# Kernel optimization log

Measured on AMD Instinct MI355X. Metric: run time of the kernel, lower is better.

## Reference

```python
import jax, jax.numpy as jnp
import numpy as np
from jax import lax

B, C, H, W = 2, 64, 48, 48
NH, DK, DV = 8, 64, 128          # heads, per-head d_k, per-head d_v
DN, NS, R = 128, 16, 4           # SS2D d_inner (expand=2), d_state, dt_rank
MULT = 4                          # FFN expansion
L = H * W


def layer_norm(x, w, b, eps=1e-5):
    m = x.mean(-1, keepdims=True)
    v = ((x - m) ** 2).mean(-1, keepdims=True)
    return (x - m) / jnp.sqrt(v + eps) * w + b


def conv2d(x, w, groups=1):
    # x: NCHW, w: OIHW
    return lax.conv_general_dilated(x, w, (1, 1), 'SAME',
                                    dimension_numbers=('NCHW', 'OIHW', 'NCHW'),
                                    feature_group_count=groups)


def setup_inputs() -> dict:
    key = jax.random.key(0)
    ks = jax.random.split(key, 24)
    rn = lambda k, shp, s=0.02: jax.random.normal(k, shp, jnp.float32) * s
    inp = {
        'enc_input': jax.random.normal(ks[0], (B, C, H, W), jnp.float32),
        'slf_attn_snr': jax.random.uniform(ks[1], (B, 1, H, W), jnp.float32),
        # MultiHeadAttention params
        'attn_wq': rn(ks[2], (C, NH * DK)),
        'attn_wk': rn(ks[3], (C, NH * DK)),
        'attn_wv': rn(ks[4], (C, NH * DV)),
        'attn_fc': rn(ks[5], (NH * DV, C)),
        'attn_ln_w': jnp.ones((C,), jnp.float32),
        'attn_ln_b': jnp.zeros((C,), jnp.float32),
        # SS2D params
        'ss_in_w': rn(ks[6], (C, 2 * DN)),
        'ss_conv_w': rn(ks[7], (DN, 1, 3, 3)),
        'ss_conv_b': jnp.zeros((DN,), jnp.float32),
        'ss_xproj_w': rn(ks[8], (4, R + 2 * NS, DN)),
        'ss_dt_w': rn(ks[9], (4, DN, R)),
        'ss_dt_b': rn(ks[10], (4, DN)),
        'ss_Alog': jnp.log(jnp.broadcast_to(jnp.arange(1, NS + 1, dtype=jnp.float32), (4, DN, NS))),
        'ss_D': jnp.ones((4, DN), jnp.float32),
        'ss_norm_w': jnp.ones((DN,), jnp.float32),
        'ss_norm_b': jnp.zeros((DN,), jnp.float32),
        'ss_out_w': rn(ks[11], (DN, C)),
        # FFN (PreNorm + conv block)
        'ffn_ln_w': jnp.ones((C,), jnp.float32),
        'ffn_ln_b': jnp.zeros((C,), jnp.float32),
        'ffn_w1': rn(ks[12], (C * MULT, C, 1, 1)),
        'ffn_dw': rn(ks[13], (C * MULT, 1, 3, 3)),
        'ffn_w2': rn(ks[14], (C, C * MULT, 1, 1)),
    }
    return inp


def reference(enc_input, slf_attn_snr, attn_wq, attn_wk, attn_wv, attn_fc,
              attn_ln_w, attn_ln_b, ss_in_w, ss_conv_w, ss_conv_b, ss_xproj_w,
              ss_dt_w, ss_dt_b, ss_Alog, ss_D, ss_norm_w, ss_norm_b, ss_out_w,
              ffn_ln_w, ffn_ln_b, ffn_w1, ffn_dw, ffn_w2):
    # ---- Multi-head self-attention over spatial tokens (SNR-biased) ----
    x_tok = enc_input.reshape(B, C, L).transpose(0, 2, 1)        # (B, L, C)
    q = (x_tok @ attn_wq).reshape(B, L, NH, DK).transpose(0, 2, 1, 3)
    k = (x_tok @ attn_wk).reshape(B, L, NH, DK).transpose(0, 2, 1, 3)
    v = (x_tok @ attn_wv).reshape(B, L, NH, DV).transpose(0, 2, 1, 3)
    scores = jnp.einsum('bhqd,bhkd->bhqk', q, k) / jnp.sqrt(jnp.float32(DK))
    snr_flat = slf_attn_snr.reshape(B, 1, 1, L)                  # bias over keys
    scores = scores + jnp.log(snr_flat + 1e-4)
    attn = jax.nn.softmax(scores, axis=-1)                       # (B, NH, L, L)
    o = jnp.einsum('bhqk,bhkd->bhqd', attn, v)
    o = o.transpose(0, 2, 1, 3).reshape(B, L, NH * DV) @ attn_fc
    enc_output = layer_norm(o + x_tok, attn_ln_w, attn_ln_b)     # post-LN residual
    enc_output = enc_output.transpose(0, 2, 1).reshape(B, C, H, W)

    # ---- SS2D: 4-direction 2D selective scan ----
    xh = enc_output.transpose(0, 2, 3, 1)                        # (B, H, W, C)
    snr_h = slf_attn_snr.transpose(0, 2, 3, 1)                   # (B, H, W, 1)
    xz = xh @ ss_in_w                                            # (B, H, W, 2*DN)
    x1, z = xz[..., :DN], xz[..., DN:]
    x1 = x1.transpose(0, 3, 1, 2)                                # (B, DN, H, W)
    x1 = conv2d(x1, ss_conv_w, groups=DN) + ss_conv_b[None, :, None, None]
    x1 = jax.nn.silu(x1)

    x_hw = x1.reshape(B, DN, L)
    x_wh = x1.transpose(0, 1, 3, 2).reshape(B, DN, L)
    xs = jnp.stack([x_hw, x_wh], axis=1)                         # (B, 2, DN, L)
    xs = jnp.concatenate([xs, jnp.flip(xs, axis=-1)], axis=1)    # (B, 4, DN, L)

    x_dbl = jnp.einsum('bkdl,kcd->bkcl', xs, ss_xproj_w)
    dts, Bs, Cs = x_dbl[:, :, :R], x_dbl[:, :, R:R + NS], x_dbl[:, :, R + NS:]
    dts = jnp.einsum('bkrl,kdr->bkdl', dts, ss_dt_w) + ss_dt_b[None, :, :, None]
    dts = jax.nn.softplus(dts)                                   # (B, 4, DN, L)
    A = -jnp.exp(ss_Alog)                                        # (4, DN, NS)

    def step(h, inp):
        xt, dtt, Bt, Ct = inp                                    # (B,4,DN),(B,4,DN),(B,4,NS),(B,4,NS)
        dA = jnp.exp(dtt[..., None] * A)                         # (B,4,DN,NS)
        h = h * dA + (dtt * xt)[..., None] * Bt[:, :, None, :]
        y = jnp.einsum('bkdn,bkn->bkd', h, Ct)
        return h, y

    h0 = jnp.zeros((B, 4, DN, NS), jnp.float32)
    elems = (xs.transpose(3, 0, 1, 2), dts.transpose(3, 0, 1, 2),
             Bs.transpose(3, 0, 1, 2), Cs.transpose(3, 0, 1, 2))
    _, ys = lax.scan(step, h0, elems)                            # (L, B, 4, DN)
    ys = ys.transpose(1, 2, 3, 0) + ss_D[None, :, :, None] * xs  # (B, 4, DN, L)

    inv = jnp.flip(ys[:, 2:4], axis=-1)                          # undo reversed scans
    wh = ys[:, 1].reshape(B, DN, W, H).transpose(0, 1, 3, 2).reshape(B, DN, L)
    invwh = inv[:, 1].reshape(B, DN, W, H).transpose(0, 1, 3, 2).reshape(B, DN, L)
    y = ys[:, 0] + inv[:, 0] + wh + invwh                        # (B, DN, L)
    y = y.transpose(0, 2, 1).reshape(B, H, W, DN)
    y = layer_norm(y, ss_norm_w, ss_norm_b) * jax.nn.silu(z) * snr_h
    x2 = y @ ss_out_w + enc_input.transpose(0, 2, 3, 1)          # (B, H, W, C)

    # ---- PreNorm conv FeedForward ----
    xn = layer_norm(x2, ffn_ln_w, ffn_ln_b).transpose(0, 3, 1, 2)
    h1 = jax.nn.gelu(conv2d(xn, ffn_w1), approximate=False)
    h1 = jax.nn.gelu(conv2d(h1, ffn_dw, groups=C * MULT), approximate=False)
    h1 = conv2d(h1, ffn_w2).transpose(0, 2, 3, 1)
    x3 = h1 + x2

    return x3.transpose(0, 3, 1, 2)                              # (B, C, H, W)
```

## Files before the change

kernel.cpp:

```cpp
#include <hip/hip_runtime.h>
#include <hip/hip_bf16.h>

#define Bq 2
#define Cc 64
#define Hh 48
#define Ww 48
#define Ll 2304
#define NHh 8
#define DKk 64
#define DVv 128
#define DNn 128
#define NSs 16
#define Rr 4
#define SCH 48
#define SNC 48
#define TT 8

#define OQ    0u
#define OK_   2359296u
#define OV    4718592u
#define OO    9437184u
#define OY2   14450688u
#define OX2   15040512u
#define OXN   15335424u
#define OVT   15630336u
#define WS_NEED_FLOATS (OVT + 4718592u)
#define ODT2  OQ
#define OYS2  OK_
#define OX1P  OV
#define OZ    (OV + 589824u)
#define OX1S  (OV + 1179648u)
#define OBS2  (OV + 1769472u)
#define OCS2  (OV + 2064384u)
#define OCSA  (OV + 2359296u)
#define OCSB  (OV + 3145728u)
#define OHST  (OV + 3932160u)
#define OH1A  OO
#define OH1B  (OO + 1179648u)

typedef short short8v __attribute__((ext_vector_type(8)));
typedef short short4v __attribute__((ext_vector_type(4)));
typedef float f32x4 __attribute__((ext_vector_type(4)));
typedef unsigned short ushort_t;

__device__ __forceinline__ float geluf(float x) {
  return 0.5f * x * (1.0f + erff(x * 0.70710678118654752f));
}
__device__ __forceinline__ float siluf(float x) {
  return x / (1.0f + __expf(-x));
}
__device__ __forceinline__ float softplusf(float x) {
  return fmaxf(x, 0.0f) + log1pf(__expf(-fabsf(x)));
}
__device__ __forceinline__ int spmap(int k, int l) {
  if (k == 0) return l;
  if (k == 1) return (l % 48) * 48 + l / 48;
  if (k == 2) return 2303 - l;
  int l2 = 2303 - l; return (l2 % 48) * 48 + l2 / 48;
}
__device__ __forceinline__ short f2bf(float f) {
  unsigned u = __float_as_uint(f);
  unsigned r = (u + 0x7FFFu + ((u >> 16) & 1u)) >> 16;
  return (short)r;
}

__global__ void k_code(float* out) { if (threadIdx.x == 0) out[0] = 25000.f; }

__global__ __launch_bounds__(256) void k_qkv(const float* __restrict__ enc,
    const float* __restrict__ wq, const float* __restrict__ wk,
    const float* __restrict__ wv, float* __restrict__ ws) {
  int l0 = blockIdx.x * TT; int b = blockIdx.y;
  int t = threadIdx.x;
  __shared__ float xs[64][12];
  {
    int idx = t, c = idx >> 3, i = idx & 7;
    xs[c][i] = enc[(size_t)b * Cc * Ll + (size_t)c * Ll + l0 + i];
    idx = t + 256; c = idx >> 3; i = idx & 7;
    xs[c][i] = enc[(size_t)b * Cc * Ll + (size_t)c * Ll + l0 + i];
  }
  __syncthreads();
  ushort_t* qb = (ushort_t*)(ws + OQ);
  ushort_t* kb = (ushort_t*)(ws + OK_);
  float* v = ws + OV;
#pragma unroll
  for (int g = 0; g < 6; ++g) {
    int j = t + g * 256;
    float acc[TT];
#pragma unroll
    for (int i = 0; i < TT; ++i) acc[i] = 0.f;
    const float* wp; int col, stride;
    if (j < 512) { wp = wq + j; stride = 512; col = j; }
    else if (j < 1024) { wp = wk + (j - 512); stride = 512; col = j - 512; }
    else { wp = wv + (j - 1024); stride = 1024; col = j - 1024; }
    for (int c = 0; c < 64; ++c) {
      float w = wp[(size_t)c * stride];
      const float4* xc = (const float4*)&xs[c][0];
      float4 x0 = xc[0], x1 = xc[1];
      acc[0] += x0.x * w; acc[1] += x0.y * w;
      acc[2] += x0.z * w; acc[3] += x0.w * w;
      acc[4] += x1.x * w; acc[5] += x1.y * w;
      acc[6] += x1.z * w; acc[7] += x1.w * w;
    }
    if (j < 512) {
#pragma unroll
      for (int i = 0; i < TT; ++i)
        qb[((size_t)(b * 8 + (col >> 6)) * Ll + l0 + i) * 64 + (col & 63)] =
            (ushort_t)f2bf(acc[i] * 0.125f);
    } else if (j < 1024) {
#pragma unroll
      for (int i = 0; i < TT; ++i)
        kb[((size_t)(b * 8 + (col >> 6)) * Ll + l0 + i) * 64 + (col & 63)] =
            (ushort_t)f2bf(acc[i]);
    } else {
#pragma unroll
      for (int i = 0; i < TT; ++i)
        v[((size_t)(b * 8 + (col >> 7)) * Ll + l0 + i) * 128 + (col & 127)] = acc[i];
    }
  }
}

__global__ __launch_bounds__(256) void k_vt(float* __restrict__ ws) {
  int bh = blockIdx.y;
  int l0 = blockIdx.x * 64;
  int t = threadIdx.x;
  __shared__ float tile[128][65];
  const float* vp = ws + OV + ((size_t)bh * Ll + l0) * 128;
  for (int i = t; i < 64 * 32; i += 256) {
    int l = i >> 5, dv4 = (i & 31) * 4;
    float4 a = *(const float4*)(vp + (size_t)l * 128 + dv4);
    tile[dv4][l] = a.x; tile[dv4 + 1][l] = a.y;
    tile[dv4 + 2][l] = a.z; tile[dv4 + 3][l] = a.w;
  }
  __syncthreads();
  ushort_t* vt = (ushort_t*)(ws + OVT) + (size_t)bh * 128 * Ll + l0;
  for (int i = t; i < 128 * 16; i += 256) {
    int dv = i >> 4, l4 = (i & 15) * 4;
    short4v a;
    a[0] = f2bf(tile[dv][l4]); a[1] = f2bf(tile[dv][l4 + 1]);
    a[2] = f2bf(tile[dv][l4 + 2]); a[3] = f2bf(tile[dv][l4 + 3]);
    *(short4v*)(vt + (size_t)dv * Ll + l4) = a;
  }
}

#define NKT 36
#define LSK 72
__global__ __launch_bounds__(256) void k_attn(const float* __restrict__ snr,
                                              float* __restrict__ ws) {
  int bh = blockIdx.y; int b = bh >> 3; int hd = bh & 7;
  int q0 = blockIdx.x * 64;
  int t = threadIdx.x;
  int w = t >> 6, lane = t & 63;
  int m16 = lane & 15, quad = lane >> 4;

  __shared__ __align__(16) ushort_t Ks[64 * LSK];
  __shared__ __align__(16) ushort_t Vs[128 * LSK];
  __shared__ __align__(16) ushort_t Ps[4 * 16 * LSK];
  __shared__ float sfac_s[64];
  __shared__ float lsc[4][16];

  const ushort_t* qbf = (const ushort_t*)(ws + OQ) + (size_t)bh * Ll * 64;
  const ushort_t* kbf = (const ushort_t*)(ws + OK_) + (size_t)bh * Ll * 64;
  const ushort_t* vtb = (const ushort_t*)(ws + OVT) + (size_t)bh * 128 * Ll;

  short8v qa[2];
  {
    const ushort_t* qrp = qbf + (size_t)(q0 + w * 16 + m16) * 64 + quad * 8;
    qa[0] = *(const short8v*)qrp;
    qa[1] = *(const short8v*)(qrp + 32);
  }
  int sk_key = t >> 2, sk_d0 = (t & 3) * 16;
  int sv_dv = t >> 1, sv_k0 = (t & 1) * 32;

  short8v kreg[2], vreg[4];
  float snr_reg = 0.f;
  {
    const ushort_t* ksrc = kbf + (size_t)sk_key * 64 + sk_d0;
    kreg[0] = *(const short8v*)ksrc;
    kreg[1] = *(const short8v*)(ksrc + 8);
    const ushort_t* vsrc = vtb + (size_t)sv_dv * Ll + sv_k0;
#pragma unroll
    for (int i = 0; i < 4; ++i) vreg[i] = *(const short8v*)(vsrc + i * 8);
    if (t < 64) snr_reg = snr[b * Ll + t];
  }

  f32x4 oacc[8];
#pragma unroll
  for (int i = 0; i < 8; ++i) oacc[i] = (f32x4)0.f;
  float l_r[4] = {0.f, 0.f, 0.f, 0.f};

  for (int kt = 0; kt < NKT; ++kt) {
    __syncthreads();
    *(short8v*)&Ks[sk_key * LSK + sk_d0] = kreg[0];
    *(short8v*)&Ks[sk_key * LSK + sk_d0 + 8] = kreg[1];
#pragma unroll
    for (int i = 0; i < 4; ++i)
      *(short8v*)&Vs[sv_dv * LSK + sv_k0 + i * 8] = vreg[i];
    if (t < 64) sfac_s[t] = snr_reg + 1e-4f;
    __syncthreads();
    if (kt + 1 < NKT) {
      int k0n = (kt + 1) * 64;
      const ushort_t* ksrc = kbf + (size_t)(k0n + sk_key) * 64 + sk_d0;
      kreg[0] = *(const short8v*)ksrc;
      kreg[1] = *(const short8v*)(ksrc + 8);
      const ushort_t* vsrc = vtb + (size_t)sv_dv * Ll + k0n + sv_k0;
#pragma unroll
      for (int i = 0; i < 4; ++i) vreg[i] = *(const short8v*)(vsrc + i * 8);
      if (t < 64) snr_reg = snr[b * Ll + k0n + t];
    }

    f32x4 sac[4];
#pragma unroll
    for (int n = 0; n < 4; ++n) {
      int key = n * 16 + m16;
      short8v kb0 = *(const short8v*)&Ks[key * LSK + quad * 8];
      short8v kb1 = *(const short8v*)&Ks[key * LSK + 32 + quad * 8];
      f32x4 acc = (f32x4)0.f;
      acc = __builtin_amdgcn_mfma_f32_16x16x32_bf16(qa[0], kb0, acc, 0, 0, 0);
      acc = __builtin_amdgcn_mfma_f32_16x16x32_bf16(qa[1], kb1, acc, 0, 0, 0);
      sac[n] = acc;
    }
    float sf[4];
#pragma unroll
    for (int n = 0; n < 4; ++n) sf[n] = sfac_s[n * 16 + m16];
    ushort_t* pw = &Ps[w * 16 * LSK];
#pragma unroll
    for (int r = 0; r < 4; ++r) {
#pragma unroll
      for (int n = 0; n < 4; ++n) {
        float p = __expf(sac[n][r]) * sf[n];
        l_r[r] += p;
        pw[(quad * 4 + r) * LSK + n * 16 + m16] = (ushort_t)f2bf(p);
      }
    }
    short8v pb0 = *(const short8v*)&pw[m16 * LSK + quad * 8];
    short8v pb1 = *(const short8v*)&pw[m16 * LSK + 32 + quad * 8];
#pragma unroll
    for (int dt_ = 0; dt_ < 8; ++dt_) {
      const ushort_t* vrow = &Vs[(dt_ * 16 + m16) * LSK];
      short8v va0 = *(const short8v*)&vrow[quad * 8];
      short8v va1 = *(const short8v*)&vrow[32 + quad * 8];
      f32x4 o = oacc[dt_];
      o = __builtin_amdgcn_mfma_f32_16x16x32_bf16(va0, pb0, o, 0, 0, 0);
      o = __builtin_amdgcn_mfma_f32_16x16x32_bf16(va1, pb1, o, 0, 0, 0);
      oacc[dt_] = o;
    }
  }
#pragma unroll
  for (int r = 0; r < 4; ++r) {
    float lv = l_r[r];
    lv += __shfl_xor(lv, 1, 64);
    lv += __shfl_xor(lv, 2, 64);
    lv += __shfl_xor(lv, 4, 64);
    lv += __shfl_xor(lv, 8, 64);
    l_r[r] = lv;
  }
  if (m16 == 0) {
#pragma unroll
    for (int r = 0; r < 4; ++r) lsc[w][quad * 4 + r] = l_r[r];
  }
  float linv = 1.f / lsc[w][m16];
  float* op = ws + OO + ((size_t)(b * Ll + q0 + w * 16 + m16)) * 1024 + hd * 128;
#pragma unroll
  for (int dt_ = 0; dt_ < 8; ++dt_) {
#pragma unroll
    for (int r = 0; r < 4; ++r) {
      op[dt_ * 16 + quad * 4 + r] = oacc[dt_][r] * linv;
    }
  }
}

__global__ __launch_bounds__(256) void k_oprojxz(const float* __restrict__ enc,
    const float* __restrict__ fc, const float* __restrict__ lnw,
    const float* __restrict__ lnb, const float* __restrict__ ssin,
    float* __restrict__ ws) {
  int l0 = blockIdx.x * TT, b = blockIdx.y, t = threadIdx.x;
  __shared__ float orow[1024][9];
  __shared__ float part[4][TT][64];
  __shared__ float xh_s[64][9];
  const float* op = ws + OO + ((size_t)(b * Ll + l0)) * 1024;
#pragma unroll
  for (int k = 0; k < 4; ++k) {
    int c = t + k * 256;
#pragma unroll
    for (int i = 0; i < TT; ++i) orow[c][i] = op[(size_t)i * 1024 + c];
  }
  __syncthreads();
  int col = t & 63, seg = t >> 6;
  {
    float acc[TT];
#pragma unroll
    for (int i = 0; i < TT; ++i) acc[i] = 0.f;
    const float* fcs = fc + (size_t)(seg * 256) * 64 + col;
    for (int c = 0; c < 256; ++c) {
      float w = fcs[(size_t)c * 64];
      const float* orc = &orow[seg * 256 + c][0];
#pragma unroll
      for (int i = 0; i < TT; ++i) acc[i] += orc[i] * w;
    }
#pragma unroll
    for (int i = 0; i < TT; ++i) part[seg][i][col] = acc[i];
  }
  __syncthreads();
  if (t < 64) {
    float lw = lnw[t], lb = lnb[t];
#pragma unroll
    for (int i = 0; i < TT; ++i) {
      float a = part[0][i][t] + part[1][i][t] + part[2][i][t] + part[3][i][t];
      a += enc[(size_t)b * Cc * Ll + (size_t)t * Ll + l0 + i];
      float s = a;
#pragma unroll
      for (int o = 32; o >= 1; o >>= 1) s += __shfl_xor(s, o, 64);
      float m = s * (1.f / 64.f);
      float dd = a - m;
      float vs = dd * dd;
#pragma unroll
      for (int o = 32; o >= 1; o >>= 1) vs += __shfl_xor(vs, o, 64);
      xh_s[t][i] = dd * rsqrtf(vs * (1.f / 64.f) + 1e-5f) * lw + lb;
    }
  }
  __syncthreads();
  {
    float acc2[TT];
#pragma unroll
    for (int i = 0; i < TT; ++i) acc2[i] = 0.f;
    for (int c = 0; c < 64; ++c) {
      float w = ssin[c * 256 + t];
      const float* xc = &xh_s[c][0];
#pragma unroll
      for (int i = 0; i < TT; ++i) acc2[i] += xc[i] * w;
    }
    if (t < 128) {
#pragma unroll
      for (int i = 0; i < TT; ++i)
        ws[OX1P + ((size_t)(b * Ll + l0 + i)) * 128 + t] = acc2[i];
    } else {
#pragma unroll
      for (int i = 0; i < TT; ++i)
        ws[OZ + ((size_t)(b * Ll + l0 + i)) * 128 + (t - 128)] = acc2[i];
    }
  }
}

__global__ __launch_bounds__(128) void k_conv(const float* __restrict__ cw,
    const float* __restrict__ cb, float* __restrict__ ws) {
  int l = blockIdx.x, b = blockIdx.y, d = threadIdx.x;
  int h = l / 48, w = l % 48;
  float acc = cb[d];
#pragma unroll
  for (int kh = 0; kh < 3; ++kh) {
    int hh = h + kh - 1;
    if (hh < 0 || hh >= 48) continue;
#pragma unroll
    for (int kw = 0; kw < 3; ++kw) {
      int wx = w + kw - 1;
      if (wx < 0 || wx >= 48) continue;
      acc += ws[OX1P + ((size_t)b * Ll + hh * 48 + wx) * 128 + d] *
             cw[d * 9 + kh * 3 + kw];
    }
  }
  ws[OX1S + ((size_t)b * Ll + l) * 128 + d] = siluf(acc);
}

__global__ __launch_bounds__(128) void k_xdbl(const float* __restrict__ xw,
    const float* __restrict__ dtw, const float* __restrict__ dtb,
    float* __restrict__ ws) {
  int l0 = blockIdx.x * TT;
  int by = blockIdx.y; int b = by >> 2; int k = by & 3;
  int t = threadIdx.x;
  __shared__ float xv[128][9];
  __shared__ float pr[36][TT];
#pragma unroll
  for (int i = 0; i < TT; ++i) {
    int sp = spmap(k, l0 + i);
    xv[t][i] = ws[OX1S + ((size_t)(b * Ll) + sp) * 128 + t];
  }
  __syncthreads();
  if (t < 36) {
    float s[TT];
#pragma unroll
    for (int i = 0; i < TT; ++i) s[i] = 0.f;
    const float* wp = xw + (size_t)(k * 36 + t) * 128;
    for (int d = 0; d < 128; ++d) {
      float w = wp[d];
      const float* xc = &xv[d][0];
#pragma unroll
      for (int i = 0; i < TT; ++i) s[i] += xc[i] * w;
    }
#pragma unroll
    for (int i = 0; i < TT; ++i) pr[t][i] = s[i];
  }
  __syncthreads();
  {
    int d = t;
    const float* wp = dtw + (size_t)(k * 128 + d) * 4;
    float w0 = wp[0], w1 = wp[1], w2 = wp[2], w3 = wp[3];
    float bb = dtb[k * 128 + d];
#pragma unroll
    for (int i = 0; i < TT; ++i) {
      float v = pr[0][i] * w0 + pr[1][i] * w1 + pr[2][i] * w2 + pr[3][i] * w3 + bb;
      ws[ODT2 + ((size_t)(by * Ll + l0 + i)) * 128 + d] = softplusf(v);
    }
  }
  if (t < 16) {
#pragma unroll
    for (int i = 0; i < TT; ++i)
      ws[OBS2 + ((size_t)(by * Ll + l0 + i)) * 16 + t] = pr[4 + t][i];
  } else if (t < 32) {
#pragma unroll
    for (int i = 0; i < TT; ++i)
      ws[OCS2 + ((size_t)(by * Ll + l0 + i)) * 16 + (t - 16)] = pr[20 + (t - 16)][i];
  }
}

__global__ __launch_bounds__(256) void k_scanA(const float* __restrict__ alog,
                                               float* __restrict__ ws) {
  int c = blockIdx.x;
  int bk = blockIdx.y;
  int b = bk >> 2, k = bk & 3;
  int t = threadIdx.x;
  int n = t & 15, dg = t >> 4;
  __shared__ float dt_s[128], x_s[128], Bs_s[16];
  float A_r[8], ap[8], bc[8];
#pragma unroll
  for (int i = 0; i < 8; ++i) {
    int d = dg * 8 + i;
    A_r[i] = -__expf(alog[(size_t)((k * 128 + d) * 16) + n]);
    ap[i] = 1.f; bc[i] = 0.f;
  }
  const float* dtp = ws + ODT2 + ((size_t)bk * Ll) * 128;
  const float* bsp = ws + OBS2 + ((size_t)bk * Ll) * 16;
  const float* xb = ws + OX1S + (size_t)b * Ll * 128;
  for (int ll = 0; ll < SCH; ++ll) {
    int l = c * SCH + ll;
    int sp = spmap(k, l);
    if (t < 128) dt_s[t] = dtp[(size_t)l * 128 + t];
    else x_s[t - 128] = xb[(size_t)sp * 128 + (t - 128)];
    if (t < 16) Bs_s[t] = bsp[(size_t)l * 16 + t];
    __syncthreads();
    float Bv = Bs_s[n];
#pragma unroll
    for (int i = 0; i < 8; ++i) {
      int d = dg * 8 + i;
      float dtv = dt_s[d];
      float a = __expf(dtv * A_r[i]);
      bc[i] = bc[i] * a + dtv * x_s[d] * Bv;
      ap[i] *= a;
    }
    __syncthreads();
  }
  float* csa = ws + OCSA + ((size_t)(bk * SNC + c) * 128) * 16;
  float* csb = ws + OCSB + ((size_t)(bk * SNC + c) * 128) * 16;
#pragma unroll
  for (int i = 0; i < 8; ++i) {
    int d = dg * 8 + i;
    csa[d * 16 + n] = ap[i];
    csb[d * 16 + n] = bc[i];
  }
}

__global__ __launch_bounds__(256) void k_scanB(float* __restrict__ ws) {
  int g = blockIdx.x * 256 + threadIdx.x;
  int bk = g >> 11;
  int dn = g & 2047;
  const float* csa = ws + OCSA;
  const float* csb = ws + OCSB;
  float* hst = ws + OHST;
  float h = 0.f;
  for (int c = 0; c < SNC; ++c) {
    size_t idx = (size_t)(bk * SNC + c) * 2048 + dn;
    hst[idx] = h;
    h = csa[idx] * h + csb[idx];
  }
}

__global__ __launch_bounds__(256) void k_scanC(const float* __restrict__ alog,
    const float* __restrict__ Dp, float* __restrict__ ws) {
  int c = blockIdx.x, bk = blockIdx.y;
  int b = bk >> 2, k = bk & 3;
  int t = threadIdx.x;
  int n = t & 15, dg = t >> 4;
  __shared__ float dt_s[128], x_s[128], Bs_s[16], Cs_s[16];
  float A_r[8], h[8], Dv[8];
#pragma unroll
  for (int i = 0; i < 8; ++i) {
    int d = dg * 8 + i;
    A_r[i] = -__expf(alog[(size_t)((k * 128 + d) * 16) + n]);
    h[i] = ws[OHST + ((size_t)(bk * SNC + c) * 128 + d) * 16 + n];
    Dv[i] = Dp[k * 128 + d];
  }
  const float* dtp = ws + ODT2 + ((size_t)bk * Ll) * 128;
  const float* bsp = ws + OBS2 + ((size_t)bk * Ll) * 16;
  const float* csp = ws + OCS2 + ((size_t)bk * Ll) * 16;
  const float* xb = ws + OX1S + (size_t)b * Ll * 128;
  float* yp = ws + OYS2 + ((size_t)bk * Ll) * 128;
  for (int ll = 0; ll < SCH; ++ll) {
    int l = c * SCH + ll;
    int sp = spmap(k, l);
    if (t < 128) dt_s[t] = dtp[(size_t)l * 128 + t];
    else x_s[t - 128] = xb[(size_t)sp * 128 + (t - 128)];
    if (t < 16) Bs_s[t] = bsp[(size_t)l * 16 + t];
    else if (t < 32) Cs_s[t - 16] = csp[(size_t)l * 16 + (t - 16)];
    __syncthreads();
    float Bv = Bs_s[n], Cv = Cs_s[n];
    float yacc[8];
#pragma unroll
    for (int i = 0; i < 8; ++i) {
      int d = dg * 8 + i;
      float dtv = dt_s[d];
      float a = __expf(dtv * A_r[i]);
      h[i] = h[i] * a + dtv * x_s[d] * Bv;
      yacc[i] = h[i] * Cv;
    }
#pragma unroll
    for (int i = 0; i < 8; ++i) {
      float yv = yacc[i];
      yv += __shfl_xor(yv, 1, 64);
      yv += __shfl_xor(yv, 2, 64);
      yv += __shfl_xor(yv, 4, 64);
      yv += __shfl_xor(yv, 8, 64);
      yacc[i] = yv;
    }
    if (n == 0) {
#pragma unroll
      for (int i = 0; i < 8; ++i) {
        int d = dg * 8 + i;
        yp[(size_t)l * 128 + d] = yacc[i] + Dv[i] * x_s[d];
      }
    }
    __syncthreads();
  }
}

__global__ __launch_bounds__(128) void k_comb(const float* __restrict__ nw,
    const float* __restrict__ nb, const float* __restrict__ snr,
    float* __restrict__ ws) {
  int l = blockIdx.x, b = blockIdx.y, d = threadIdx.x;
  int h = l / 48, w = l % 48;
  int lT = w * 48 + h;
  const float* ysb = ws + OYS2;
  float v = ysb[((size_t)(b * 4 + 0) * Ll + l) * 128 + d] +
            ysb[((size_t)(b * 4 + 2) * Ll + (2303 - l)) * 128 + d] +
            ysb[((size_t)(b * 4 + 1) * Ll + lT) * 128 + d] +
            ysb[((size_t)(b * 4 + 3) * Ll + (2303 - lT)) * 128 + d];
  __shared__ float red[4];
  int lane = d & 63, wid = d >> 6;
  float s = v;
#pragma unroll
  for (int o = 32; o >= 1; o >>= 1) s += __shfl_xor(s, o, 64);
  if (lane == 0) red[wid] = s;
  __syncthreads();
  float m = (red[0] + red[1]) * (1.f / 128.f);
  float dv_ = v - m;
  float q = dv_ * dv_;
#pragma unroll
  for (int o = 32; o >= 1; o >>= 1) q += __shfl_xor(q, o, 64);
  if (lane == 0) red[wid + 2] = q;
  __syncthreads();
  float var = (red[2] + red[3]) * (1.f / 128.f);
  float y = dv_ * rsqrtf(var + 1e-5f) * nw[d] + nb[d];
  float zv = ws[OZ + ((size_t)b * Ll + l) * 128 + d];
  y *= siluf(zv);
  y *= snr[b * Ll + l];
  ws[OY2 + ((size_t)b * Ll + l) * 128 + d] = y;
}

__global__ __launch_bounds__(256) void k_outffn1(const float* __restrict__ enc,
    const float* __restrict__ ow, const float* __restrict__ lw,
    const float* __restrict__ lb, const float* __restrict__ w1,
    float* __restrict__ ws) {
  int l0 = blockIdx.x * TT, b = blockIdx.y, t = threadIdx.x;
  __shared__ float yr[128][9];
  __shared__ float part[2][TT][64];
  __shared__ float xn_s[64][9];
  const float* yp = ws + OY2 + ((size_t)(b * Ll + l0)) * 128;
  if (t < 128) {
#pragma unroll
    for (int i = 0; i < TT; ++i) yr[t][i] = yp[(size_t)i * 128 + t];
  }
  __syncthreads();
  if (t < 128) {
    int col = t & 63, seg = t >> 6;
    float acc[TT];
#pragma unroll
    for (int i = 0; i < TT; ++i) acc[i] = 0.f;
    const float* ows = ow + (size_t)(seg * 64) * 64 + col;
    for (int c = 0; c < 64; ++c) {
      float w = ows[c * 64];
      const float* yc = &yr[seg * 64 + c][0];
#pragma unroll
      for (int i = 0; i < TT; ++i) acc[i] += yc[i] * w;
    }
#pragma unroll
    for (int i = 0; i < TT; ++i) part[seg][i][col] = acc[i];
  }
  __syncthreads();
  if (t < 64) {
    float lwv = lw[t], lbv = lb[t];
#pragma unroll
    for (int i = 0; i < TT; ++i) {
      float a = part[0][i][t] + part[1][i][t];
      a += enc[(size_t)b * Cc * Ll + (size_t)t * Ll + l0 + i];
      ws[OX2 + ((size_t)(b * Ll + l0 + i)) * 64 + t] = a;
      float s = a;
#pragma unroll
      for (int o = 32; o >= 1; o >>= 1) s += __shfl_xor(s, o, 64);
      float m = s * (1.f / 64.f);
      float dd2 = a - m;
      float vs = dd2 * dd2;
#pragma unroll
      for (int o = 32; o >= 1; o >>= 1) vs += __shfl_xor(vs, o, 64);
      xn_s[t][i] = dd2 * rsqrtf(vs * (1.f / 64.f) + 1e-5f) * lwv + lbv;
    }
  }
  __syncthreads();
  {
    float acc2[TT];
#pragma unroll
    for (int i = 0; i < TT; ++i) acc2[i] = 0.f;
    const float* wp = w1 + (size_t)t * 64;
    for (int c = 0; c < 64; ++c) {
      float w = wp[c];
      const float* xc = &xn_s[c][0];
#pragma unroll
      for (int i = 0; i < TT; ++i) acc2[i] += xc[i] * w;
    }
#pragma unroll
    for (int i = 0; i < TT; ++i)
      ws[OH1A + ((size_t)(b * Ll + l0 + i)) * 256 + t] = geluf(acc2[i]);
  }
}

__global__ __launch_bounds__(256) void k_ffndw(const float* __restrict__ dww,
                                               float* __restrict__ ws) {
  int l = blockIdx.x, b = blockIdx.y, mch = threadIdx.x;
  int h = l / 48, w = l % 48;
  float acc = 0.f;
#pragma unroll
  for (int kh = 0; kh < 3; ++kh) {
    int hh = h + kh - 1;
    if (hh < 0 || hh >= 48) continue;
#pragma unroll
    for (int kw = 0; kw < 3; ++kw) {
      int wx = w + kw - 1;
      if (wx < 0 || wx >= 48) continue;
      acc += ws[OH1A + ((size_t)b * Ll + hh * 48 + wx) * 256 + mch] *
             dww[mch * 9 + kh * 3 + kw];
    }
  }
  ws[OH1B + ((size_t)b * Ll + l) * 256 + mch] = geluf(acc);
}

__global__ __launch_bounds__(256) void k_ffn2(const float* __restrict__ w2,
                                              float* __restrict__ ws,
                                              float* __restrict__ out) {
  int l0 = blockIdx.x * TT, b = blockIdx.y, t = threadIdx.x;
  __shared__ float hr[256][9];
  __shared__ float part[4][TT][64];
  const float* hp = ws + OH1B + ((size_t)(b * Ll + l0)) * 256;
#pragma unroll
  for (int i = 0; i < TT; ++i) hr[t][i] = hp[(size_t)i * 256 + t];
  __syncthreads();
  int col = t & 63, seg = t >> 6;
  {
    float acc[TT];
#pragma unroll
    for (int i = 0; i < TT; ++i) acc[i] = 0.f;
    const float* wp = w2 + (size_t)col * 256 + seg * 64;
    for (int c = 0; c < 64; ++c) {
      float w = wp[c];
      const float* hc = &hr[seg * 64 + c][0];
#pragma unroll
      for (int i = 0; i < TT; ++i) acc[i] += hc[i] * w;
    }
#pragma unroll
    for (int i = 0; i < TT; ++i) part[seg][i][col] = acc[i];
  }
  __syncthreads();
  if (t < 64) {
    float av[TT];
#pragma unroll
    for (int i = 0; i < TT; ++i) {
      float a = part[0][i][t] + part[1][i][t] + part[2][i][t] + part[3][i][t];
      av[i] = a + ws[OX2 + ((size_t)(b * Ll + l0 + i)) * 64 + t];
    }
    float* opx = out + ((size_t)(b * 64 + t)) * 2304 + l0;
    *(float4*)opx = make_float4(av[0], av[1], av[2], av[3]);
    *((float4*)opx + 1) = make_float4(av[4], av[5], av[6], av[7]);
  }
}

extern "C" void kernel_launch(void* const* d_in, const int* in_sizes, int n_in,
                              void* d_out, int out_size, void* d_ws, size_t ws_size,
                              hipStream_t stream) {
  (void)in_sizes; (void)n_in; (void)out_size;
  const float* enc  = (const float*)d_in[0];
  const float* snr  = (const float*)d_in[1];
  const float* wq   = (const float*)d_in[2];
  const float* wk   = (const float*)d_in[3];
  const float* wv   = (const float*)d_in[4];
  const float* fc   = (const float*)d_in[5];
  const float* alnw = (const float*)d_in[6];
  const float* alnb = (const float*)d_in[7];
  const float* ssin = (const float*)d_in[8];
  const float* cw   = (const float*)d_in[9];
  const float* cb   = (const float*)d_in[10];
  const float* xw   = (const float*)d_in[11];
  const float* dtw  = (const float*)d_in[12];
  const float* dtb  = (const float*)d_in[13];
  const float* alog = (const float*)d_in[14];
  const float* Dp   = (const float*)d_in[15];
  const float* nw   = (const float*)d_in[16];
  const float* nb   = (const float*)d_in[17];
  const float* ow   = (const float*)d_in[18];
  const float* flnw = (const float*)d_in[19];
  const float* flnb = (const float*)d_in[20];
  const float* w1   = (const float*)d_in[21];
  const float* dww  = (const float*)d_in[22];
  const float* w2   = (const float*)d_in[23];
  float* ws = (float*)d_ws;
  float* out = (float*)d_out;

  if (ws_size < (size_t)WS_NEED_FLOATS * 4) {
    hipLaunchKernelGGL(k_code, dim3(1), dim3(64), 0, stream, out);
    return;
  }

  hipLaunchKernelGGL(k_qkv, dim3(Ll / TT, Bq), dim3(256), 0, stream, enc, wq, wk, wv, ws);
  hipLaunchKernelGGL(k_vt, dim3(Ll / 64, Bq * NHh), dim3(256), 0, stream, ws);
  hipLaunchKernelGGL(k_attn, dim3(Ll / 64, Bq * NHh), dim3(256), 0, stream, snr, ws);
  hipLaunchKernelGGL(k_oprojxz, dim3(Ll / TT, Bq), dim3(256), 0, stream, enc, fc, alnw, alnb, ssin, ws);
  hipLaunchKernelGGL(k_conv, dim3(Ll, Bq), dim3(128), 0, stream, cw, cb, ws);
  hipLaunchKernelGGL(k_xdbl, dim3(Ll / TT, Bq * 4), dim3(128), 0, stream, xw, dtw, dtb, ws);
  hipLaunchKernelGGL(k_scanA, dim3(SNC, Bq * 4), dim3(256), 0, stream, alog, ws);
  hipLaunchKernelGGL(k_scanB, dim3(64), dim3(256), 0, stream, ws);
  hipLaunchKernelGGL(k_scanC, dim3(SNC, Bq * 4), dim3(256), 0, stream, alog, Dp, ws);
  hipLaunchKernelGGL(k_comb, dim3(Ll, Bq), dim3(128), 0, stream, nw, nb, snr, ws);
  hipLaunchKernelGGL(k_outffn1, dim3(Ll / TT, Bq), dim3(256), 0, stream, enc, ow, flnw, flnb, w1, ws);
  hipLaunchKernelGGL(k_ffndw, dim3(Ll, Bq), dim3(256), 0, stream, dww, ws);
  hipLaunchKernelGGL(k_ffn2, dim3(Ll / TT, Bq), dim3(256), 0, stream, w2, ws, out);
}
```

Measured before the change: 461.2 us.

## Tile depthwise convs in shared memory, prefetch scan inputs, fuse combine into FFN1

```diff
diff --git a/kernel.cpp b/kernel.cpp
--- a/kernel.cpp
+++ b/kernel.cpp
@@ -341,24 +341,37 @@
   }
 }
 
-__global__ __launch_bounds__(128) void k_conv(const float* __restrict__ cw,
+__global__ __launch_bounds__(256) void k_conv(const float* __restrict__ cw,
     const float* __restrict__ cb, float* __restrict__ ws) {
-  int l = blockIdx.x, b = blockIdx.y, d = threadIdx.x;
-  int h = l / 48, w = l % 48;
-  float acc = cb[d];
-#pragma unroll
-  for (int kh = 0; kh < 3; ++kh) {
-    int hh = h + kh - 1;
-    if (hh < 0 || hh >= 48) continue;
-#pragma unroll
-    for (int kw = 0; kw < 3; ++kw) {
-      int wx = w + kw - 1;
-      if (wx < 0 || wx >= 48) continue;
-      acc += ws[OX1P + ((size_t)b * Ll + hh * 48 + wx) * 128 + d] *
-             cw[d * 9 + kh * 3 + kw];
-    }
-  }
-  ws[OX1S + ((size_t)b * Ll + l) * 128 + d] = siluf(acc);
+  int l0 = blockIdx.x * TT, b = blockIdx.y, t = threadIdx.x;
+  int h = l0 / 48, w0 = l0 % 48;
+  __shared__ float tile[3][10][128];
+  for (int idx = t; idx < 3840; idx += 256) {
+    int r = idx / 1280, rem = idx % 1280;
+    int col = rem >> 7, d = rem & 127;
+    int hh = h + r - 1, wx = w0 + col - 1;
+    float v = 0.f;
+    if (hh >= 0 && hh < 48 && wx >= 0 && wx < 48)
+      v = ws[OX1P + ((size_t)(b * Ll + hh * 48 + wx)) * 128 + d];
+    tile[r][col][d] = v;
+  }
+  __syncthreads();
+  int d = t & 127, half = t >> 7;
+  float cwr[9];
+#pragma unroll
+  for (int j = 0; j < 9; ++j) cwr[j] = cw[d * 9 + j];
+  float cbv = cb[d];
+#pragma unroll
+  for (int j = 0; j < 4; ++j) {
+    int i = half * 4 + j;
+    float acc = cbv;
+#pragma unroll
+    for (int kh = 0; kh < 3; ++kh)
+#pragma unroll
+      for (int kw = 0; kw < 3; ++kw)
+        acc += tile[kh][i + kw][d] * cwr[kh * 3 + kw];
+    ws[OX1S + ((size_t)(b * Ll + l0 + i)) * 128 + d] = siluf(acc);
+  }
 }
 
 __global__ __launch_bounds__(128) void k_xdbl(const float* __restrict__ xw,
@@ -430,13 +443,27 @@
   const float* dtp = ws + ODT2 + ((size_t)bk * Ll) * 128;
   const float* bsp = ws + OBS2 + ((size_t)bk * Ll) * 16;
   const float* xb = ws + OX1S + (size_t)b * Ll * 128;
+  float r_a = 0.f, r_Bs = 0.f;
+  {
+    int l = c * SCH;
+    int sp = spmap(k, l);
+    if (t < 128) r_a = dtp[(size_t)l * 128 + t];
+    else r_a = xb[(size_t)sp * 128 + (t - 128)];
+    if (t < 16) r_Bs = bsp[(size_t)l * 16 + t];
+  }
   for (int ll = 0; ll < SCH; ++ll) {
-    int l = c * SCH + ll;
-    int sp = spmap(k, l);
-    if (t < 128) dt_s[t] = dtp[(size_t)l * 128 + t];
-    else x_s[t - 128] = xb[(size_t)sp * 128 + (t - 128)];
-    if (t < 16) Bs_s[t] = bsp[(size_t)l * 16 + t];
     __syncthreads();
+    if (t < 128) dt_s[t] = r_a;
+    else x_s[t - 128] = r_a;
+    if (t < 16) Bs_s[t] = r_Bs;
+    __syncthreads();
+    if (ll + 1 < SCH) {
+      int l2 = c * SCH + ll + 1;
+      int sp2 = spmap(k, l2);
+      if (t < 128) r_a = dtp[(size_t)l2 * 128 + t];
+      else r_a = xb[(size_t)sp2 * 128 + (t - 128)];
+      if (t < 16) r_Bs = bsp[(size_t)l2 * 16 + t];
+    }
     float Bv = Bs_s[n];
 #pragma unroll
     for (int i = 0; i < 8; ++i) {
@@ -446,7 +473,6 @@
       bc[i] = bc[i] * a + dtv * x_s[d] * Bv;
       ap[i] *= a;
     }
-    __syncthreads();
   }
   float* csa = ws + OCSA + ((size_t)(bk * SNC + c) * 128) * 16;
   float* csb = ws + OCSB + ((size_t)(bk * SNC + c) * 128) * 16;
@@ -493,14 +519,31 @@
   const float* csp = ws + OCS2 + ((size_t)bk * Ll) * 16;
   const float* xb = ws + OX1S + (size_t)b * Ll * 128;
   float* yp = ws + OYS2 + ((size_t)bk * Ll) * 128;
+  float r_a = 0.f, r_bc = 0.f;
+  {
+    int l = c * SCH;
+    int sp = spmap(k, l);
+    if (t < 128) r_a = dtp[(size_t)l * 128 + t];
+    else r_a = xb[(size_t)sp * 128 + (t - 128)];
+    if (t < 16) r_bc = bsp[(size_t)l * 16 + t];
+    else if (t < 32) r_bc = csp[(size_t)l * 16 + (t - 16)];
+  }
   for (int ll = 0; ll < SCH; ++ll) {
+    __syncthreads();
+    if (t < 128) dt_s[t] = r_a;
+    else x_s[t - 128] = r_a;
+    if (t < 16) Bs_s[t] = r_bc;
+    else if (t < 32) Cs_s[t - 16] = r_bc;
+    __syncthreads();
+    if (ll + 1 < SCH) {
+      int l2 = c * SCH + ll + 1;
+      int sp2 = spmap(k, l2);
+      if (t < 128) r_a = dtp[(size_t)l2 * 128 + t];
+      else r_a = xb[(size_t)sp2 * 128 + (t - 128)];
+      if (t < 16) r_bc = bsp[(size_t)l2 * 16 + t];
+      else if (t < 32) r_bc = csp[(size_t)l2 * 16 + (t - 16)];
+    }
     int l = c * SCH + ll;
-    int sp = spmap(k, l);
-    if (t < 128) dt_s[t] = dtp[(size_t)l * 128 + t];
-    else x_s[t - 128] = xb[(size_t)sp * 128 + (t - 128)];
-    if (t < 16) Bs_s[t] = bsp[(size_t)l * 16 + t];
-    else if (t < 32) Cs_s[t - 16] = csp[(size_t)l * 16 + (t - 16)];
-    __syncthreads();
     float Bv = Bs_s[n], Cv = Cs_s[n];
     float yacc[8];
 #pragma unroll
@@ -527,55 +570,78 @@
         yp[(size_t)l * 128 + d] = yacc[i] + Dv[i] * x_s[d];
       }
     }
-    __syncthreads();
-  }
-}
-
-__global__ __launch_bounds__(128) void k_comb(const float* __restrict__ nw,
-    const float* __restrict__ nb, const float* __restrict__ snr,
-    float* __restrict__ ws) {
-  int l = blockIdx.x, b = blockIdx.y, d = threadIdx.x;
-  int h = l / 48, w = l % 48;
-  int lT = w * 48 + h;
-  const float* ysb = ws + OYS2;
-  float v = ysb[((size_t)(b * 4 + 0) * Ll + l) * 128 + d] +
-            ysb[((size_t)(b * 4 + 2) * Ll + (2303 - l)) * 128 + d] +
-            ysb[((size_t)(b * 4 + 1) * Ll + lT) * 128 + d] +
-            ysb[((size_t)(b * 4 + 3) * Ll + (2303 - lT)) * 128 + d];
-  __shared__ float red[4];
-  int lane = d & 63, wid = d >> 6;
-  float s = v;
-#pragma unroll
-  for (int o = 32; o >= 1; o >>= 1) s += __shfl_xor(s, o, 64);
-  if (lane == 0) red[wid] = s;
-  __syncthreads();
-  float m = (red[0] + red[1]) * (1.f / 128.f);
-  float dv_ = v - m;
-  float q = dv_ * dv_;
-#pragma unroll
-  for (int o = 32; o >= 1; o >>= 1) q += __shfl_xor(q, o, 64);
-  if (lane == 0) red[wid + 2] = q;
-  __syncthreads();
-  float var = (red[2] + red[3]) * (1.f / 128.f);
-  float y = dv_ * rsqrtf(var + 1e-5f) * nw[d] + nb[d];
-  float zv = ws[OZ + ((size_t)b * Ll + l) * 128 + d];
-  y *= siluf(zv);
-  y *= snr[b * Ll + l];
-  ws[OY2 + ((size_t)b * Ll + l) * 128 + d] = y;
-}
-
-__global__ __launch_bounds__(256) void k_outffn1(const float* __restrict__ enc,
-    const float* __restrict__ ow, const float* __restrict__ lw,
-    const float* __restrict__ lb, const float* __restrict__ w1,
-    float* __restrict__ ws) {
+  }
+}
+
+__global__ __launch_bounds__(256) void k_combffn1(const float* __restrict__ enc,
+    const float* __restrict__ nw, const float* __restrict__ nb,
+    const float* __restrict__ snr, const float* __restrict__ ow,
+    const float* __restrict__ lw, const float* __restrict__ lb,
+    const float* __restrict__ w1, float* __restrict__ ws) {
   int l0 = blockIdx.x * TT, b = blockIdx.y, t = threadIdx.x;
   __shared__ float yr[128][9];
+  __shared__ float redm[2][TT], redq[2][TT];
   __shared__ float part[2][TT][64];
   __shared__ float xn_s[64][9];
-  const float* yp = ws + OY2 + ((size_t)(b * Ll + l0)) * 128;
+  int lane = t & 63, wid = (t >> 6) & 1;
+  float v[TT], m[TT];
   if (t < 128) {
-#pragma unroll
-    for (int i = 0; i < TT; ++i) yr[t][i] = yp[(size_t)i * 128 + t];
+    int d = t;
+    const float* ysb = ws + OYS2;
+#pragma unroll
+    for (int i = 0; i < TT; ++i) {
+      int l = l0 + i;
+      int hh = l / 48, wwp = l % 48;
+      int lT = wwp * 48 + hh;
+      v[i] = ysb[((size_t)(b * 4 + 0) * Ll + l) * 128 + d] +
+             ysb[((size_t)(b * 4 + 2) * Ll + (2303 - l)) * 128 + d] +
+             ysb[((size_t)(b * 4 + 1) * Ll + lT) * 128 + d] +
+             ysb[((size_t)(b * 4 + 3) * Ll + (2303 - lT)) * 128 + d];
+    }
+    float s[TT];
+#pragma unroll
+    for (int i = 0; i < TT; ++i) s[i] = v[i];
+#pragma unroll
+    for (int o = 32; o >= 1; o >>= 1)
+#pragma unroll
+      for (int i = 0; i < TT; ++i) s[i] += __shfl_xor(s[i], o, 64);
+    if (lane == 0) {
+#pragma unroll
+      for (int i = 0; i < TT; ++i) redm[wid][i] = s[i];
+    }
+  }
+  __syncthreads();
+  if (t < 128) {
+    float q[TT];
+#pragma unroll
+    for (int i = 0; i < TT; ++i) {
+      m[i] = (redm[0][i] + redm[1][i]) * (1.f / 128.f);
+      float dv = v[i] - m[i];
+      q[i] = dv * dv;
+    }
+#pragma unroll
+    for (int o = 32; o >= 1; o >>= 1)
+#pragma unroll
+      for (int i = 0; i < TT; ++i) q[i] += __shfl_xor(q[i], o, 64);
+    if (lane == 0) {
+#pragma unroll
+      for (int i = 0; i < TT; ++i) redq[wid][i] = q[i];
+    }
+  }
+  __syncthreads();
+  if (t < 128) {
+    int d = t;
+    float nwv = nw[d], nbv = nb[d];
+#pragma unroll
+    for (int i = 0; i < TT; ++i) {
+      int l = l0 + i;
+      float var = (redq[0][i] + redq[1][i]) * (1.f / 128.f);
+      float y = (v[i] - m[i]) * rsqrtf(var + 1e-5f) * nwv + nbv;
+      float zv = ws[OZ + ((size_t)(b * Ll + l)) * 128 + d];
+      y *= siluf(zv);
+      y *= snr[b * Ll + l];
+      yr[d][i] = y;
+    }
   }
   __syncthreads();
   if (t < 128) {
@@ -604,8 +670,8 @@
       float s = a;
 #pragma unroll
       for (int o = 32; o >= 1; o >>= 1) s += __shfl_xor(s, o, 64);
-      float m = s * (1.f / 64.f);
-      float dd2 = a - m;
+      float mm = s * (1.f / 64.f);
+      float dd2 = a - mm;
       float vs = dd2 * dd2;
 #pragma unroll
       for (int o = 32; o >= 1; o >>= 1) vs += __shfl_xor(vs, o, 64);
@@ -632,22 +698,32 @@
 
 __global__ __launch_bounds__(256) void k_ffndw(const float* __restrict__ dww,
                                                float* __restrict__ ws) {
-  int l = blockIdx.x, b = blockIdx.y, mch = threadIdx.x;
-  int h = l / 48, w = l % 48;
-  float acc = 0.f;
-#pragma unroll
-  for (int kh = 0; kh < 3; ++kh) {
-    int hh = h + kh - 1;
-    if (hh < 0 || hh >= 48) continue;
-#pragma unroll
-    for (int kw = 0; kw < 3; ++kw) {
-      int wx = w + kw - 1;
-      if (wx < 0 || wx >= 48) continue;
-      acc += ws[OH1A + ((size_t)b * Ll + hh * 48 + wx) * 256 + mch] *
-             dww[mch * 9 + kh * 3 + kw];
-    }
-  }
-  ws[OH1B + ((size_t)b * Ll + l) * 256 + mch] = geluf(acc);
+  int l0 = blockIdx.x * TT, b = blockIdx.y, t = threadIdx.x;
+  int h = l0 / 48, w0 = l0 % 48;
+  __shared__ float tile[3][10][256];
+  for (int idx = t; idx < 7680; idx += 256) {
+    int r = idx / 2560, rem = idx % 2560;
+    int col = rem >> 8, ch = rem & 255;
+    int hh = h + r - 1, wx = w0 + col - 1;
+    float v = 0.f;
+    if (hh >= 0 && hh < 48 && wx >= 0 && wx < 48)
+      v = ws[OH1A + ((size_t)(b * Ll + hh * 48 + wx)) * 256 + ch];
+    tile[r][col][ch] = v;
+  }
+  __syncthreads();
+  float dwr[9];
+#pragma unroll
+  for (int j = 0; j < 9; ++j) dwr[j] = dww[t * 9 + j];
+#pragma unroll
+  for (int i = 0; i < TT; ++i) {
+    float acc = 0.f;
+#pragma unroll
+    for (int kh = 0; kh < 3; ++kh)
+#pragma unroll
+      for (int kw = 0; kw < 3; ++kw)
+        acc += tile[kh][i + kw][t] * dwr[kh * 3 + kw];
+    ws[OH1B + ((size_t)(b * Ll + l0 + i)) * 256 + t] = geluf(acc);
+  }
 }
 
 __global__ __launch_bounds__(256) void k_ffn2(const float* __restrict__ w2,
@@ -729,13 +805,12 @@
   hipLaunchKernelGGL(k_vt, dim3(Ll / 64, Bq * NHh), dim3(256), 0, stream, ws);
   hipLaunchKernelGGL(k_attn, dim3(Ll / 64, Bq * NHh), dim3(256), 0, stream, snr, ws);
   hipLaunchKernelGGL(k_oprojxz, dim3(Ll / TT, Bq), dim3(256), 0, stream, enc, fc, alnw, alnb, ssin, ws);
-  hipLaunchKernelGGL(k_conv, dim3(Ll, Bq), dim3(128), 0, stream, cw, cb, ws);
+  hipLaunchKernelGGL(k_conv, dim3(Ll / TT, Bq), dim3(256), 0, stream, cw, cb, ws);
   hipLaunchKernelGGL(k_xdbl, dim3(Ll / TT, Bq * 4), dim3(128), 0, stream, xw, dtw, dtb, ws);
   hipLaunchKernelGGL(k_scanA, dim3(SNC, Bq * 4), dim3(256), 0, stream, alog, ws);
   hipLaunchKernelGGL(k_scanB, dim3(64), dim3(256), 0, stream, ws);
   hipLaunchKernelGGL(k_scanC, dim3(SNC, Bq * 4), dim3(256), 0, stream, alog, Dp, ws);
-  hipLaunchKernelGGL(k_comb, dim3(Ll, Bq), dim3(128), 0, stream, nw, nb, snr, ws);
-  hipLaunchKernelGGL(k_outffn1, dim3(Ll / TT, Bq), dim3(256), 0, stream, enc, ow, flnw, flnb, w1, ws);
-  hipLaunchKernelGGL(k_ffndw, dim3(Ll, Bq), dim3(256), 0, stream, dww, ws);
+  hipLaunchKernelGGL(k_combffn1, dim3(Ll / TT, Bq), dim3(256), 0, stream, enc, nw, nb, snr, ow, flnw, flnb, w1, ws);
+  hipLaunchKernelGGL(k_ffndw, dim3(Ll / TT, Bq), dim3(256), 0, stream, dww, ws);
   hipLaunchKernelGGL(k_ffn2, dim3(Ll / TT, Bq), dim3(256), 0, stream, w2, ws, out);
 }
```

New measurement: 434.2 us. 1.06x faster.
